# Optimization experiments

Measured on AMD Instinct MI355X. Metric: run time of the kernel, lower is better.

Reference implementation:

```python
import jax, jax.numpy as jnp
import numpy as np

BS, N, D, B, D_PM = 8, 4096, 1024, 8, 64
BUDGET = 16.0


def setup_inputs() -> dict:
    key = jax.random.key(0)
    ks = jax.random.split(key, 6)
    H = jax.random.normal(ks[0], (BS, N, D), jnp.float32)
    surprise = jax.random.normal(ks[1], (BS, N, D), jnp.float32)
    # W_pm initialized as (1/B)*I + small noise, as in initialize()
    eye = jnp.eye(D_PM, dtype=jnp.float32)
    W_pm = eye / B + 0.01 * jax.random.normal(ks[2], (BS, B, D_PM, D_PM), jnp.float32)
    proj_in_w = jax.random.normal(ks[3], (D_PM, D), jnp.float32) / np.float32(np.sqrt(D))
    proj_in_b = jnp.zeros((D_PM,), jnp.float32)
    # original zero-inits proj_out; use small values so output is non-trivial
    proj_out_w = 0.02 * jax.random.normal(ks[4], (D, D_PM), jnp.float32)
    proj_out_b = jnp.zeros((D,), jnp.float32)
    raw_beta = jnp.full((B,), -3.0, jnp.float32)
    raw_decay = jnp.full((B,), np.float32(np.log(0.999 / 0.001)), jnp.float32)  # logit(0.999)
    surp_scale = jnp.ones((1,), jnp.float32)
    surp_bias = jnp.zeros((1,), jnp.float32)
    return dict(H=H, surprise=surprise, W_pm=W_pm,
                proj_in_w=proj_in_w, proj_in_b=proj_in_b,
                proj_out_w=proj_out_w, proj_out_b=proj_out_b,
                raw_beta=raw_beta, raw_decay=raw_decay,
                surp_scale=surp_scale, surp_bias=surp_bias)


def reference(H, surprise, W_pm, proj_in_w, proj_in_b, proj_out_w, proj_out_b,
              raw_beta, raw_decay, surp_scale, surp_bias):
    # ---- read ----
    pre = jnp.einsum('bnd,pd->bnp', H, proj_in_w) + proj_in_b          # [BS,N,D_pm]
    W_sum = jnp.sum(W_pm, axis=1)                                      # [BS,D_pm,D_pm]
    post = jnp.einsum('bnp,bqp->bnq', pre, W_sum)                      # pre @ W_sum^T
    pm_read = jnp.einsum('bnq,dq->bnd', post, proj_out_w) + proj_out_b # [BS,N,D]
    # ---- commit (Hebbian, surprise-gated) ----
    surp_mag = jnp.linalg.norm(surprise, axis=-1)                      # [BS,N]
    s = jax.nn.sigmoid(surp_scale * surp_mag + surp_bias)              # [BS,N]
    weighted = jnp.sqrt(s)[..., None] * pre                            # [BS,N,D_pm]
    G = jnp.einsum('bnp,bnq->bpq', weighted, weighted) / N             # [BS,D_pm,D_pm]
    beta = jax.nn.softplus(raw_beta)                                   # [B]
    decay = jax.nn.sigmoid(raw_decay)                                  # [B]
    eye = jnp.eye(D_PM, dtype=pre.dtype)
    T = decay[None, :, None, None] * eye + beta[None, :, None, None] * G[:, None]  # [BS,B,D_pm,D_pm]
    W_new = jnp.einsum('bkij,bkjq->bkiq', W_pm, T)                     # [BS,B,D_pm,D_pm]
    frob = jnp.sqrt(jnp.sum(W_new * W_new, axis=(-2, -1), keepdims=True))
    scale = jnp.minimum(BUDGET / jnp.maximum(frob, 1e-8), 1.0)
    W_new = W_new * scale
    return pm_read, W_new
```

## Files before the change

### kernel.cpp

```cpp
#include <hip/hip_runtime.h>

typedef unsigned short u16;
typedef unsigned int u32;
typedef __attribute__((ext_vector_type(4))) float f32x4;
typedef __attribute__((ext_vector_type(8))) short s16x8;

static constexpr int N_ = 4096;
static constexpr int D_ = 1024;

#define WAITV(N) asm volatile("s_waitcnt vmcnt(" #N ")" ::: "memory")
#define MEMCLOB() asm volatile("" ::: "memory")

__device__ __forceinline__ u16 f2bf(float f) {
  unsigned u = __float_as_uint(f);
  u += 0x7FFFu + ((u >> 16) & 1u);
  return (u16)(u >> 16);
}

__device__ __forceinline__ f32x4 zero4() {
  f32x4 z; z[0] = 0.f; z[1] = 0.f; z[2] = 0.f; z[3] = 0.f; return z;
}

__device__ __forceinline__ void gload16(const void* g, void* lds) {
  __builtin_amdgcn_global_load_lds(
      (const __attribute__((address_space(1))) u32*)g,
      (__attribute__((address_space(3))) u32*)lds, 16, 0, 0);
}

__global__ __launch_bounds__(256) void k_aux(
    const float* __restrict__ Wpm, const float* __restrict__ piw,
    const float* __restrict__ pw, const float* __restrict__ Sur,
    const float* __restrict__ sscale_p, const float* __restrict__ sbias_p,
    u16* __restrict__ WpB, u16* __restrict__ MB, float* __restrict__ sqs_ws) {
  __shared__ float Ws[64][65];
  int bid = blockIdx.x, tid = threadIdx.x;
  if (bid < 16) {
    size_t i0 = (size_t)bid * 4096;
    for (int idx = tid; idx < 4096; idx += 256)
      WpB[i0 + idx] = f2bf(piw[i0 + idx]);
    return;
  }
  if (bid < 144) {
    int idx2 = bid - 16;
    int b = idx2 >> 4, t = idx2 & 15;
    for (int idx = tid; idx < 4096; idx += 256) {
      float s = 0.f;
#pragma unroll
      for (int k = 0; k < 8; ++k)
        s += Wpm[((size_t)(b * 8 + k)) * 4096 + idx];
      Ws[idx >> 6][idx & 63] = s;
    }
    __syncthreads();
    u16* mb = MB + ((size_t)b << 16);
    for (int oidx = tid; oidx < 4096; oidx += 256) {
      int r = oidx >> 6, c = oidx & 63;
      int drow = t * 64 + r;
      const float* prow = pw + (size_t)drow * 64;
      float acc = 0.f;
#pragma unroll 8
      for (int q = 0; q < 64; ++q) acc += prow[q] * Ws[q][c];
      mb[(size_t)drow * 64 + c] = f2bf(acc);
    }
    return;
  }
  int w = tid >> 6, lane = tid & 63;
  int fr = (bid - 144) * 16 + w * 4;
  const float4* r0 = (const float4*)(Sur + (size_t)fr * 1024) + lane;
  float s0 = 0.f, s1 = 0.f, s2 = 0.f, s3 = 0.f;
#pragma unroll
  for (int c = 0; c < 4; ++c) {
    float4 v0 = r0[c * 64];
    float4 v1 = r0[256 + c * 64];
    float4 v2 = r0[512 + c * 64];
    float4 v3 = r0[768 + c * 64];
    s0 += v0.x * v0.x + v0.y * v0.y + v0.z * v0.z + v0.w * v0.w;
    s1 += v1.x * v1.x + v1.y * v1.y + v1.z * v1.z + v1.w * v1.w;
    s2 += v2.x * v2.x + v2.y * v2.y + v2.z * v2.z + v2.w * v2.w;
    s3 += v3.x * v3.x + v3.y * v3.y + v3.z * v3.z + v3.w * v3.w;
  }
#pragma unroll
  for (int m = 1; m < 64; m <<= 1) {
    s0 += __shfl_xor(s0, m, 64);
    s1 += __shfl_xor(s1, m, 64);
    s2 += __shfl_xor(s2, m, 64);
    s3 += __shfl_xor(s3, m, 64);
  }
  float res = s0;
  if (lane == 1) res = s1;
  if (lane == 2) res = s2;
  if (lane == 3) res = s3;
  if (lane < 4) {
    float mag = sqrtf(res);
    float s = 1.f / (1.f + __expf(-(sscale_p[0] * mag + sbias_p[0])));
    sqs_ws[fr + lane] = sqrtf(s);
  }
}

__global__ __launch_bounds__(512, 4) void k_main(
    const float* __restrict__ H, const float* __restrict__ pib,
    const float* __restrict__ pob, const u16* __restrict__ WpB,
    const u16* __restrict__ MB, const float* __restrict__ sqs_ws,
    float* __restrict__ Gpart, float* __restrict__ out) {
  __shared__ __align__(16) char arena[32768];
  __shared__ __align__(16) u16 preRP[64][72];
  __shared__ __align__(16) u16 wRPT[64][72];
  __shared__ float pobL[1024];

  const int tid = threadIdx.x;
  const int lane = tid & 63;
  const int w = tid >> 6;
  const int wm = w & 3;
  const int wk = w >> 2;
  const int llo = lane & 15;
  const int lhi = lane >> 4;
  const int b = blockIdx.x >> 6;
  const int row0 = (blockIdx.x & 63) * 64;

  float bias_t[4];
#pragma unroll
  for (int t = 0; t < 4; ++t) bias_t[t] = pib[t * 16 + llo];
  float sqs_r[4];
#pragma unroll
  for (int r = 0; r < 4; ++r)
    sqs_r[r] = sqs_ws[b * 4096 + row0 + wm * 16 + lhi * 4 + r];

  const int srow = 8 * w + (lane >> 3);
  const int sc16 = (lane & 7) ^ (srow & 7);

  f32x4 accA[4];
#pragma unroll
  for (int t = 0; t < 4; ++t) accA[t] = zero4();

  const float* hsrc = H + ((size_t)b * N_ + row0 + srow) * D_ + sc16 * 4;
  const u16* wpb = WpB + (size_t)wk * 512 + lhi * 8;

  s16x8 B0[4], B1[4];
  auto LOADB = [&](int kc, s16x8* Bs) {
#pragma unroll
    for (int t = 0; t < 4; ++t)
      Bs[t] = *(const s16x8*)(wpb + (size_t)(t * 16 + llo) * 1024 + kc * 32);
  };
  auto STAGEH = [&](int kc, int buf) {
    gload16(hsrc + kc * 32, arena + buf * 16384 + w * 1024);
    gload16(hsrc + 512 + kc * 32, arena + buf * 16384 + 8192 + w * 1024);
  };
  const int arow = wm * 16 + llo;
  const int r7a = arow & 7;
  auto COMPA = [&](int buf, const s16x8* Bs) {
    const char* abase = arena + buf * 16384 + wk * 8192 + arow * 128;
    f32x4 alo = *(const f32x4*)(abase + (((lhi * 2) ^ r7a) * 16));
    f32x4 ahi = *(const f32x4*)(abase + (((lhi * 2 + 1) ^ r7a) * 16));
    s16x8 af;
    af[0] = (short)f2bf(alo[0]); af[1] = (short)f2bf(alo[1]);
    af[2] = (short)f2bf(alo[2]); af[3] = (short)f2bf(alo[3]);
    af[4] = (short)f2bf(ahi[0]); af[5] = (short)f2bf(ahi[1]);
    af[6] = (short)f2bf(ahi[2]); af[7] = (short)f2bf(ahi[3]);
#pragma unroll
    for (int t = 0; t < 4; ++t)
      accA[t] = __builtin_amdgcn_mfma_f32_16x16x32_bf16(af, Bs[t], accA[t], 0, 0, 0);
  };

  LOADB(0, B0); STAGEH(0, 0);
  MEMCLOB();
  LOADB(1, B1); STAGEH(1, 1);
  MEMCLOB();

  for (int kc = 0; kc < 16; kc += 2) {
    WAITV(6);
    __builtin_amdgcn_s_barrier();
    COMPA(0, B0);
    MEMCLOB();
    __builtin_amdgcn_s_barrier();
    if (kc + 2 < 16) { LOADB(kc + 2, B0); STAGEH(kc + 2, 0); }
    MEMCLOB();
    if (kc + 1 == 15) { WAITV(0); } else { WAITV(6); }
    __builtin_amdgcn_s_barrier();
    COMPA(1, B1);
    MEMCLOB();
    __builtin_amdgcn_s_barrier();
    if (kc + 3 < 16) { LOADB(kc + 3, B1); STAGEH(kc + 3, 1); }
    MEMCLOB();
  }

  __syncthreads();
  float (*preF)[65] = (float(*)[65])arena;
  if (wk == 1) {
#pragma unroll
    for (int t = 0; t < 4; ++t)
#pragma unroll
      for (int r = 0; r < 4; ++r)
        preF[wm * 16 + lhi * 4 + r][t * 16 + llo] = accA[t][r];
  }
  __syncthreads();
  if (wk == 0) {
#pragma unroll
    for (int t = 0; t < 4; ++t)
#pragma unroll
      for (int r = 0; r < 4; ++r) {
        int row = wm * 16 + lhi * 4 + r;
        float v = accA[t][r] + preF[row][t * 16 + llo] + bias_t[t];
        preRP[row][t * 16 + llo] = f2bf(v);
        wRPT[t * 16 + llo][row] = f2bf(v * sqs_r[r]);
      }
  }
  __syncthreads();

  {
    f32x4 accG[4];
#pragma unroll
    for (int t = 0; t < 4; ++t) accG[t] = zero4();
    s16x8 ag = *(const s16x8*)&wRPT[wm * 16 + llo][wk * 32 + lhi * 8];
#pragma unroll
    for (int t = 0; t < 4; ++t) {
      s16x8 bg = *(const s16x8*)&wRPT[t * 16 + llo][wk * 32 + lhi * 8];
      accG[t] = __builtin_amdgcn_mfma_f32_16x16x32_bf16(ag, bg, accG[t], 0, 0, 0);
    }
    float* gout = Gpart + ((size_t)blockIdx.x * 2 + wk) * 4096;
#pragma unroll
    for (int t = 0; t < 4; ++t)
#pragma unroll
      for (int r = 0; r < 4; ++r)
        gout[(wm * 16 + lhi * 4 + r) * 64 + t * 16 + llo] = accG[t][r];
  }

  pobL[tid] = pob[tid];
  pobL[tid + 512] = pob[tid + 512];
  __syncthreads();

  const u16* mbb = MB + ((size_t)b << 16);
  const u16* msrc0 = mbb + (size_t)srow * 64 + sc16 * 8;
  auto STAGED = [&](int c, int buf) {
    gload16(msrc0 + (size_t)c * 64 * 64, arena + buf * 16384 + w * 1024);
    gload16(msrc0 + (size_t)(512 + c * 64) * 64, arena + buf * 16384 + 8192 + w * 1024);
  };
  s16x8 ad0 = *(const s16x8*)&preRP[wm * 16 + llo][lhi * 8];
  s16x8 ad1 = *(const s16x8*)&preRP[wm * 16 + llo][32 + lhi * 8];
  float* orow = out + ((size_t)b * N_ + row0 + wm * 16) * D_;

  STAGED(0, 0);
  MEMCLOB();
  STAGED(1, 1);
  MEMCLOB();
  for (int c = 0; c < 8; ++c) {
    if (c == 0) { WAITV(2); }
    else if (c == 7) { WAITV(16); }
    else { WAITV(18); }
    __builtin_amdgcn_s_barrier();
    {
      const char* dbase = arena + (c & 1) * 16384 + wk * 8192;
#pragma unroll
      for (int i = 0; i < 4; ++i) {
        int row = i * 16 + llo;
        int r7 = row & 7;
        const char* base = dbase + row * 128;
        s16x8 b0 = *(const s16x8*)(base + ((lhi ^ r7) * 16));
        s16x8 b1 = *(const s16x8*)(base + (((4 + lhi) ^ r7) * 16));
        f32x4 acc = zero4();
        acc = __builtin_amdgcn_mfma_f32_16x16x32_bf16(ad0, b0, acc, 0, 0, 0);
        acc = __builtin_amdgcn_mfma_f32_16x16x32_bf16(ad1, b1, acc, 0, 0, 0);
        int n0 = wk * 512 + c * 64 + i * 16;
        float bias = pobL[n0 + llo];
#pragma unroll
        for (int r = 0; r < 4; ++r)
          orow[(size_t)(lhi * 4 + r) * D_ + n0 + llo] = acc[r] + bias;
      }
    }
    MEMCLOB();
    __builtin_amdgcn_s_barrier();
    if (c + 2 < 8) STAGED(c + 2, c & 1);
    MEMCLOB();
  }
}

__global__ __launch_bounds__(256) void k_wnew(
    const float* __restrict__ Wpm, const float* __restrict__ Gpart,
    const float* __restrict__ rbeta, const float* __restrict__ rdecay,
    float* __restrict__ outW) {
  __shared__ float Wk[64][68];
  __shared__ float Gl[64][68];
  __shared__ float red[4];
  int bk = blockIdx.x;
  int b = bk >> 3, k = bk & 7;
  int tid = threadIdx.x;
  f32x4 a0 = zero4(), a1 = zero4(), a2 = zero4(), a3 = zero4();
  const float* gp = Gpart + (size_t)b * 128 * 4096 + tid * 16;
#pragma unroll 2
  for (int sl = 0; sl < 128; ++sl) {
    const f32x4* p = (const f32x4*)(gp + (size_t)sl * 4096);
    a0 += p[0]; a1 += p[1]; a2 += p[2]; a3 += p[3];
  }
  {
    float* gl = &Gl[tid >> 2][(tid & 3) * 16];
#pragma unroll
    for (int j = 0; j < 4; ++j) {
      gl[j] = a0[j]; gl[4 + j] = a1[j]; gl[8 + j] = a2[j]; gl[12 + j] = a3[j];
    }
  }
  const float* wsrc = Wpm + (size_t)bk * 4096;
  for (int idx = tid; idx < 4096; idx += 256)
    Wk[idx >> 6][idx & 63] = wsrc[idx];
  __syncthreads();
  float beta = log1pf(__expf(rbeta[k]));
  float decay = 1.f / (1.f + __expf(-rdecay[k]));
  float bn = beta * (1.f / 4096.f);
  int q = tid & 63;
  int rbase = tid >> 6;
  float vals[16];
  float ss = 0.f;
#pragma unroll
  for (int i = 0; i < 16; ++i) {
    int row = i * 4 + rbase;
    float acc = 0.f;
#pragma unroll 8
    for (int j = 0; j < 64; ++j) acc += Wk[row][j] * Gl[j][q];
    float v = decay * Wk[row][q] + bn * acc;
    vals[i] = v;
    ss += v * v;
  }
#pragma unroll
  for (int m = 1; m < 64; m <<= 1) ss += __shfl_xor(ss, m, 64);
  if ((tid & 63) == 0) red[tid >> 6] = ss;
  __syncthreads();
  float frob = sqrtf(red[0] + red[1] + red[2] + red[3]);
  float scale = fminf(16.f / fmaxf(frob, 1e-8f), 1.f);
  float* dst = outW + (size_t)bk * 4096;
#pragma unroll
  for (int i = 0; i < 16; ++i) dst[i * 256 + tid] = vals[i] * scale;
}

extern "C" void kernel_launch(void* const* d_in, const int* in_sizes, int n_in,
                              void* d_out, int out_size, void* d_ws, size_t ws_size,
                              hipStream_t stream) {
  const float* H      = (const float*)d_in[0];
  const float* Sur    = (const float*)d_in[1];
  const float* Wpm    = (const float*)d_in[2];
  const float* piw    = (const float*)d_in[3];
  const float* pib    = (const float*)d_in[4];
  const float* pw     = (const float*)d_in[5];
  const float* pob    = (const float*)d_in[6];
  const float* rbeta  = (const float*)d_in[7];
  const float* rdecay = (const float*)d_in[8];
  const float* sscale = (const float*)d_in[9];
  const float* sbias  = (const float*)d_in[10];
  float* out = (float*)d_out;

  char* ws = (char*)d_ws;
  u16* WpB      = (u16*)(ws);
  u16* MB       = (u16*)(ws + 131072);
  float* sqs_ws = (float*)(ws + 1179648);
  float* Gpart  = (float*)(ws + 1310720);

  k_aux<<<2192, 256, 0, stream>>>(Wpm, piw, pw, Sur, sscale, sbias,
                                  WpB, MB, sqs_ws);
  k_main<<<512, 512, 0, stream>>>(H, pib, pob, WpB, MB, sqs_ws, Gpart, out);
  k_wnew<<<64, 256, 0, stream>>>(Wpm, Gpart, rbeta, rdecay,
                                 out + (size_t)8 * 4096 * 1024);
}
```

Measured before the change: 162.3 us.

## Fuse surprise norm into main kernel, deepen H pipeline, add parallel G reduction

```diff
diff --git a/kernel.cpp b/kernel.cpp
--- a/kernel.cpp
+++ b/kernel.cpp
@@ -29,9 +29,8 @@
 
 __global__ __launch_bounds__(256) void k_aux(
     const float* __restrict__ Wpm, const float* __restrict__ piw,
-    const float* __restrict__ pw, const float* __restrict__ Sur,
-    const float* __restrict__ sscale_p, const float* __restrict__ sbias_p,
-    u16* __restrict__ WpB, u16* __restrict__ MB, float* __restrict__ sqs_ws) {
+    const float* __restrict__ pw, u16* __restrict__ WpB,
+    u16* __restrict__ MB) {
   __shared__ float Ws[64][65];
   int bid = blockIdx.x, tid = threadIdx.x;
   if (bid < 16) {
@@ -40,71 +39,36 @@
       WpB[i0 + idx] = f2bf(piw[i0 + idx]);
     return;
   }
-  if (bid < 144) {
-    int idx2 = bid - 16;
-    int b = idx2 >> 4, t = idx2 & 15;
-    for (int idx = tid; idx < 4096; idx += 256) {
-      float s = 0.f;
-#pragma unroll
-      for (int k = 0; k < 8; ++k)
-        s += Wpm[((size_t)(b * 8 + k)) * 4096 + idx];
-      Ws[idx >> 6][idx & 63] = s;
-    }
-    __syncthreads();
-    u16* mb = MB + ((size_t)b << 16);
-    for (int oidx = tid; oidx < 4096; oidx += 256) {
-      int r = oidx >> 6, c = oidx & 63;
-      int drow = t * 64 + r;
-      const float* prow = pw + (size_t)drow * 64;
-      float acc = 0.f;
+  int idx2 = bid - 16;
+  int b = idx2 >> 4, t = idx2 & 15;
+  for (int idx = tid; idx < 4096; idx += 256) {
+    float s = 0.f;
+#pragma unroll
+    for (int k = 0; k < 8; ++k)
+      s += Wpm[((size_t)(b * 8 + k)) * 4096 + idx];
+    Ws[idx >> 6][idx & 63] = s;
+  }
+  __syncthreads();
+  u16* mb = MB + ((size_t)b << 16);
+  for (int oidx = tid; oidx < 4096; oidx += 256) {
+    int r = oidx >> 6, c = oidx & 63;
+    int drow = t * 64 + r;
+    const float* prow = pw + (size_t)drow * 64;
+    float acc = 0.f;
 #pragma unroll 8
-      for (int q = 0; q < 64; ++q) acc += prow[q] * Ws[q][c];
-      mb[(size_t)drow * 64 + c] = f2bf(acc);
-    }
-    return;
-  }
-  int w = tid >> 6, lane = tid & 63;
-  int fr = (bid - 144) * 16 + w * 4;
-  const float4* r0 = (const float4*)(Sur + (size_t)fr * 1024) + lane;
-  float s0 = 0.f, s1 = 0.f, s2 = 0.f, s3 = 0.f;
-#pragma unroll
-  for (int c = 0; c < 4; ++c) {
-    float4 v0 = r0[c * 64];
-    float4 v1 = r0[256 + c * 64];
-    float4 v2 = r0[512 + c * 64];
-    float4 v3 = r0[768 + c * 64];
-    s0 += v0.x * v0.x + v0.y * v0.y + v0.z * v0.z + v0.w * v0.w;
-    s1 += v1.x * v1.x + v1.y * v1.y + v1.z * v1.z + v1.w * v1.w;
-    s2 += v2.x * v2.x + v2.y * v2.y + v2.z * v2.z + v2.w * v2.w;
-    s3 += v3.x * v3.x + v3.y * v3.y + v3.z * v3.z + v3.w * v3.w;
-  }
-#pragma unroll
-  for (int m = 1; m < 64; m <<= 1) {
-    s0 += __shfl_xor(s0, m, 64);
-    s1 += __shfl_xor(s1, m, 64);
-    s2 += __shfl_xor(s2, m, 64);
-    s3 += __shfl_xor(s3, m, 64);
-  }
-  float res = s0;
-  if (lane == 1) res = s1;
-  if (lane == 2) res = s2;
-  if (lane == 3) res = s3;
-  if (lane < 4) {
-    float mag = sqrtf(res);
-    float s = 1.f / (1.f + __expf(-(sscale_p[0] * mag + sbias_p[0])));
-    sqs_ws[fr + lane] = sqrtf(s);
+    for (int q = 0; q < 64; ++q) acc += prow[q] * Ws[q][c];
+    mb[(size_t)drow * 64 + c] = f2bf(acc);
   }
 }
 
 __global__ __launch_bounds__(512, 4) void k_main(
-    const float* __restrict__ H, const float* __restrict__ pib,
-    const float* __restrict__ pob, const u16* __restrict__ WpB,
-    const u16* __restrict__ MB, const float* __restrict__ sqs_ws,
+    const float* __restrict__ H, const float* __restrict__ Sur,
+    const float* __restrict__ pib, const float* __restrict__ pob,
+    const float* __restrict__ sscale_p, const float* __restrict__ sbias_p,
+    const u16* __restrict__ WpB, const u16* __restrict__ MB,
     float* __restrict__ Gpart, float* __restrict__ out) {
-  __shared__ __align__(16) char arena[32768];
-  __shared__ __align__(16) u16 preRP[64][72];
-  __shared__ __align__(16) u16 wRPT[64][72];
-  __shared__ float pobL[1024];
+  __shared__ __align__(16) char arena[65536];
+  __shared__ float sqsL[64];
 
   const int tid = threadIdx.x;
   const int lane = tid & 63;
@@ -116,74 +80,107 @@
   const int b = blockIdx.x >> 6;
   const int row0 = (blockIdx.x & 63) * 64;
 
-  float bias_t[4];
-#pragma unroll
-  for (int t = 0; t < 4; ++t) bias_t[t] = pib[t * 16 + llo];
-  float sqs_r[4];
-#pragma unroll
-  for (int r = 0; r < 4; ++r)
-    sqs_r[r] = sqs_ws[b * 4096 + row0 + wm * 16 + lhi * 4 + r];
+  {
+    const float* sb = Sur + ((size_t)b * N_ + row0) * D_;
+    const float sscale = sscale_p[0], sbias = sbias_p[0];
+#pragma unroll
+    for (int g = 0; g < 2; ++g) {
+      const float4* r0 = (const float4*)(sb + (size_t)(w * 8 + g * 4) * D_) + lane;
+      float s0 = 0.f, s1 = 0.f, s2 = 0.f, s3 = 0.f;
+#pragma unroll
+      for (int c = 0; c < 4; ++c) {
+        float4 v0 = r0[c * 64];
+        float4 v1 = r0[256 + c * 64];
+        float4 v2 = r0[512 + c * 64];
+        float4 v3 = r0[768 + c * 64];
+        s0 += v0.x * v0.x + v0.y * v0.y + v0.z * v0.z + v0.w * v0.w;
+        s1 += v1.x * v1.x + v1.y * v1.y + v1.z * v1.z + v1.w * v1.w;
+        s2 += v2.x * v2.x + v2.y * v2.y + v2.z * v2.z + v2.w * v2.w;
+        s3 += v3.x * v3.x + v3.y * v3.y + v3.z * v3.z + v3.w * v3.w;
+      }
+#pragma unroll
+      for (int m = 1; m < 64; m <<= 1) {
+        s0 += __shfl_xor(s0, m, 64);
+        s1 += __shfl_xor(s1, m, 64);
+        s2 += __shfl_xor(s2, m, 64);
+        s3 += __shfl_xor(s3, m, 64);
+      }
+      float res = s0;
+      if (lane == 1) res = s1;
+      if (lane == 2) res = s2;
+      if (lane == 3) res = s3;
+      if (lane < 4) {
+        float mag = sqrtf(res);
+        float s = 1.f / (1.f + __expf(-(sscale * mag + sbias)));
+        sqsL[w * 8 + g * 4 + lane] = sqrtf(s);
+      }
+    }
+  }
+  __syncthreads();
 
   const int srow = 8 * w + (lane >> 3);
   const int sc16 = (lane & 7) ^ (srow & 7);
-
-  f32x4 accA[4];
-#pragma unroll
-  for (int t = 0; t < 4; ++t) accA[t] = zero4();
-
   const float* hsrc = H + ((size_t)b * N_ + row0 + srow) * D_ + sc16 * 4;
   const u16* wpb = WpB + (size_t)wk * 512 + lhi * 8;
 
-  s16x8 B0[4], B1[4];
-  auto LOADB = [&](int kc, s16x8* Bs) {
-#pragma unroll
-    for (int t = 0; t < 4; ++t)
-      Bs[t] = *(const s16x8*)(wpb + (size_t)(t * 16 + llo) * 1024 + kc * 32);
-  };
-  auto STAGEH = [&](int kc, int buf) {
-    gload16(hsrc + kc * 32, arena + buf * 16384 + w * 1024);
-    gload16(hsrc + 512 + kc * 32, arena + buf * 16384 + 8192 + w * 1024);
-  };
+  f32x4 accA[4];
+#pragma unroll
+  for (int t = 0; t < 4; ++t) accA[t] = zero4();
+  s16x8 Bf[2][4];
+
   const int arow = wm * 16 + llo;
   const int r7a = arow & 7;
-  auto COMPA = [&](int buf, const s16x8* Bs) {
-    const char* abase = arena + buf * 16384 + wk * 8192 + arow * 128;
-    f32x4 alo = *(const f32x4*)(abase + (((lhi * 2) ^ r7a) * 16));
-    f32x4 ahi = *(const f32x4*)(abase + (((lhi * 2 + 1) ^ r7a) * 16));
-    s16x8 af;
-    af[0] = (short)f2bf(alo[0]); af[1] = (short)f2bf(alo[1]);
-    af[2] = (short)f2bf(alo[2]); af[3] = (short)f2bf(alo[3]);
-    af[4] = (short)f2bf(ahi[0]); af[5] = (short)f2bf(ahi[1]);
-    af[6] = (short)f2bf(ahi[2]); af[7] = (short)f2bf(ahi[3]);
-#pragma unroll
-    for (int t = 0; t < 4; ++t)
-      accA[t] = __builtin_amdgcn_mfma_f32_16x16x32_bf16(af, Bs[t], accA[t], 0, 0, 0);
-  };
-
-  LOADB(0, B0); STAGEH(0, 0);
+
+#define STAGEH(kc)                                                          \
+  gload16(hsrc + (kc) * 32, arena + ((kc) & 3) * 16384 + w * 1024);         \
+  gload16(hsrc + 512 + (kc) * 32, arena + ((kc) & 3) * 16384 + 8192 + w * 1024)
+
+#define LOADB(kc)                                                           \
+  _Pragma("unroll") for (int t = 0; t < 4; ++t) Bf[(kc) & 1][t] =           \
+      *(const s16x8*)(wpb + (size_t)(t * 16 + llo) * 1024 + (kc) * 32)
+
+  STAGEH(0); STAGEH(1); STAGEH(2);
+  LOADB(0); LOADB(1);
   MEMCLOB();
-  LOADB(1, B1); STAGEH(1, 1);
-  MEMCLOB();
-
-  for (int kc = 0; kc < 16; kc += 2) {
-    WAITV(6);
+
+#pragma unroll
+  for (int kc = 0; kc < 16; ++kc) {
+    if (kc <= 13) { WAITV(12); }
+    else if (kc == 14) { WAITV(8); }
+    else { WAITV(0); }
     __builtin_amdgcn_s_barrier();
-    COMPA(0, B0);
     MEMCLOB();
-    __builtin_amdgcn_s_barrier();
-    if (kc + 2 < 16) { LOADB(kc + 2, B0); STAGEH(kc + 2, 0); }
+    {
+      const char* abase = arena + (kc & 3) * 16384 + wk * 8192 + arow * 128;
+      f32x4 alo = *(const f32x4*)(abase + (((lhi * 2) ^ r7a) * 16));
+      f32x4 ahi = *(const f32x4*)(abase + (((lhi * 2 + 1) ^ r7a) * 16));
+      s16x8 af;
+      af[0] = (short)f2bf(alo[0]); af[1] = (short)f2bf(alo[1]);
+      af[2] = (short)f2bf(alo[2]); af[3] = (short)f2bf(alo[3]);
+      af[4] = (short)f2bf(ahi[0]); af[5] = (short)f2bf(ahi[1]);
+      af[6] = (short)f2bf(ahi[2]); af[7] = (short)f2bf(ahi[3]);
+#pragma unroll
+      for (int t = 0; t < 4; ++t)
+        accA[t] = __builtin_amdgcn_mfma_f32_16x16x32_bf16(af, Bf[kc & 1][t],
+                                                          accA[t], 0, 0, 0);
+    }
+    if (kc + 2 < 16) { LOADB(kc + 2); }
+    if (kc + 3 < 16) { STAGEH(kc + 3); }
     MEMCLOB();
-    if (kc + 1 == 15) { WAITV(0); } else { WAITV(6); }
-    __builtin_amdgcn_s_barrier();
-    COMPA(1, B1);
-    MEMCLOB();
-    __builtin_amdgcn_s_barrier();
-    if (kc + 3 < 16) { LOADB(kc + 3, B1); STAGEH(kc + 3, 1); }
-    MEMCLOB();
-  }
+  }
+#undef STAGEH
+#undef LOADB
+
+  float bias_t[4];
+#pragma unroll
+  for (int t = 0; t < 4; ++t) bias_t[t] = pib[t * 16 + llo];
 
   __syncthreads();
   float (*preF)[65] = (float(*)[65])arena;
+  u16 (*preRP)[72] = (u16(*)[72])(arena + 18432);
+  u16 (*wRPT)[72] = (u16(*)[72])(arena + 28672);
+  float* pobL = (float*)(arena + 38912);
+
   if (wk == 1) {
 #pragma unroll
     for (int t = 0; t < 4; ++t)
@@ -200,7 +197,7 @@
         int row = wm * 16 + lhi * 4 + r;
         float v = accA[t][r] + preF[row][t * 16 + llo] + bias_t[t];
         preRP[row][t * 16 + llo] = f2bf(v);
-        wRPT[t * 16 + llo][row] = f2bf(v * sqs_r[r]);
+        wRPT[t * 16 + llo][row] = f2bf(v * sqsL[row]);
       }
   }
   __syncthreads();
@@ -222,42 +219,29 @@
       for (int r = 0; r < 4; ++r)
         gout[(wm * 16 + lhi * 4 + r) * 64 + t * 16 + llo] = accG[t][r];
   }
-
   pobL[tid] = pob[tid];
   pobL[tid + 512] = pob[tid + 512];
   __syncthreads();
 
-  const u16* mbb = MB + ((size_t)b << 16);
-  const u16* msrc0 = mbb + (size_t)srow * 64 + sc16 * 8;
-  auto STAGED = [&](int c, int buf) {
-    gload16(msrc0 + (size_t)c * 64 * 64, arena + buf * 16384 + w * 1024);
-    gload16(msrc0 + (size_t)(512 + c * 64) * 64, arena + buf * 16384 + 8192 + w * 1024);
-  };
-  s16x8 ad0 = *(const s16x8*)&preRP[wm * 16 + llo][lhi * 8];
-  s16x8 ad1 = *(const s16x8*)&preRP[wm * 16 + llo][32 + lhi * 8];
-  float* orow = out + ((size_t)b * N_ + row0 + wm * 16) * D_;
-
-  STAGED(0, 0);
-  MEMCLOB();
-  STAGED(1, 1);
-  MEMCLOB();
-  for (int c = 0; c < 8; ++c) {
-    if (c == 0) { WAITV(2); }
-    else if (c == 7) { WAITV(16); }
-    else { WAITV(18); }
-    __builtin_amdgcn_s_barrier();
-    {
-      const char* dbase = arena + (c & 1) * 16384 + wk * 8192;
+  {
+    s16x8 ad0 = *(const s16x8*)&preRP[wm * 16 + llo][lhi * 8];
+    s16x8 ad1 = *(const s16x8*)&preRP[wm * 16 + llo][32 + lhi * 8];
+    const u16* mcol = MB + ((size_t)b << 16) + (size_t)(wk * 512) * 64 + lhi * 8;
+    float* orow = out + ((size_t)b * N_ + row0 + wm * 16) * D_;
+#pragma unroll
+    for (int c = 0; c < 8; ++c) {
+      s16x8 f0[4], f1[4];
 #pragma unroll
       for (int i = 0; i < 4; ++i) {
-        int row = i * 16 + llo;
-        int r7 = row & 7;
-        const char* base = dbase + row * 128;
-        s16x8 b0 = *(const s16x8*)(base + ((lhi ^ r7) * 16));
-        s16x8 b1 = *(const s16x8*)(base + (((4 + lhi) ^ r7) * 16));
+        const u16* p = mcol + (size_t)(c * 64 + i * 16 + llo) * 64;
+        f0[i] = *(const s16x8*)p;
+        f1[i] = *(const s16x8*)(p + 32);
+      }
+#pragma unroll
+      for (int i = 0; i < 4; ++i) {
         f32x4 acc = zero4();
-        acc = __builtin_amdgcn_mfma_f32_16x16x32_bf16(ad0, b0, acc, 0, 0, 0);
-        acc = __builtin_amdgcn_mfma_f32_16x16x32_bf16(ad1, b1, acc, 0, 0, 0);
+        acc = __builtin_amdgcn_mfma_f32_16x16x32_bf16(ad0, f0[i], acc, 0, 0, 0);
+        acc = __builtin_amdgcn_mfma_f32_16x16x32_bf16(ad1, f1[i], acc, 0, 0, 0);
         int n0 = wk * 512 + c * 64 + i * 16;
         float bias = pobL[n0 + llo];
 #pragma unroll
@@ -265,40 +249,41 @@
           orow[(size_t)(lhi * 4 + r) * D_ + n0 + llo] = acc[r] + bias;
       }
     }
-    MEMCLOB();
-    __builtin_amdgcn_s_barrier();
-    if (c + 2 < 8) STAGED(c + 2, c & 1);
-    MEMCLOB();
-  }
+  }
+}
+
+__global__ __launch_bounds__(256) void k_gred(
+    const float* __restrict__ Gpart, float* __restrict__ Gsum) {
+  __shared__ float red[4][64];
+  int b = blockIdx.x >> 6, g = blockIdx.x & 63;
+  int lane = threadIdx.x & 63, q = threadIdx.x >> 6;
+  const float* src = Gpart + ((size_t)b * 128 + q * 32) * 4096 + g * 64 + lane;
+  float s = 0.f;
+#pragma unroll 8
+  for (int i = 0; i < 32; ++i) s += src[(size_t)i * 4096];
+  red[q][lane] = s;
+  __syncthreads();
+  if (q == 0)
+    Gsum[(size_t)b * 4096 + g * 64 + lane] =
+        red[0][lane] + red[1][lane] + red[2][lane] + red[3][lane];
 }
 
 __global__ __launch_bounds__(256) void k_wnew(
-    const float* __restrict__ Wpm, const float* __restrict__ Gpart,
+    const float* __restrict__ Wpm, const float* __restrict__ Gsum,
     const float* __restrict__ rbeta, const float* __restrict__ rdecay,
     float* __restrict__ outW) {
-  __shared__ float Wk[64][68];
-  __shared__ float Gl[64][68];
+  __shared__ float Wk[64][66];
+  __shared__ float Gl[64][66];
   __shared__ float red[4];
   int bk = blockIdx.x;
   int b = bk >> 3, k = bk & 7;
   int tid = threadIdx.x;
-  f32x4 a0 = zero4(), a1 = zero4(), a2 = zero4(), a3 = zero4();
-  const float* gp = Gpart + (size_t)b * 128 * 4096 + tid * 16;
-#pragma unroll 2
-  for (int sl = 0; sl < 128; ++sl) {
-    const f32x4* p = (const f32x4*)(gp + (size_t)sl * 4096);
-    a0 += p[0]; a1 += p[1]; a2 += p[2]; a3 += p[3];
-  }
-  {
-    float* gl = &Gl[tid >> 2][(tid & 3) * 16];
-#pragma unroll
-    for (int j = 0; j < 4; ++j) {
-      gl[j] = a0[j]; gl[4 + j] = a1[j]; gl[8 + j] = a2[j]; gl[12 + j] = a3[j];
-    }
-  }
   const float* wsrc = Wpm + (size_t)bk * 4096;
-  for (int idx = tid; idx < 4096; idx += 256)
+  const float* gsrc = Gsum + (size_t)b * 4096;
+  for (int idx = tid; idx < 4096; idx += 256) {
     Wk[idx >> 6][idx & 63] = wsrc[idx];
+    Gl[idx >> 6][idx & 63] = gsrc[idx];
+  }
   __syncthreads();
   float beta = log1pf(__expf(rbeta[k]));
   float decay = 1.f / (1.f + __expf(-rdecay[k]));
@@ -345,14 +330,15 @@
   float* out = (float*)d_out;
 
   char* ws = (char*)d_ws;
-  u16* WpB      = (u16*)(ws);
-  u16* MB       = (u16*)(ws + 131072);
-  float* sqs_ws = (float*)(ws + 1179648);
-  float* Gpart  = (float*)(ws + 1310720);
-
-  k_aux<<<2192, 256, 0, stream>>>(Wpm, piw, pw, Sur, sscale, sbias,
-                                  WpB, MB, sqs_ws);
-  k_main<<<512, 512, 0, stream>>>(H, pib, pob, WpB, MB, sqs_ws, Gpart, out);
-  k_wnew<<<64, 256, 0, stream>>>(Wpm, Gpart, rbeta, rdecay,
+  u16* WpB     = (u16*)(ws);
+  u16* MB      = (u16*)(ws + 131072);
+  float* Gsum  = (float*)(ws + 1179648);
+  float* Gpart = (float*)(ws + 1310720);
+
+  k_aux<<<144, 256, 0, stream>>>(Wpm, piw, pw, WpB, MB);
+  k_main<<<512, 512, 0, stream>>>(H, Sur, pib, pob, sscale, sbias,
+                                  WpB, MB, Gpart, out);
+  k_gred<<<512, 256, 0, stream>>>(Gpart, Gsum);
+  k_wnew<<<64, 256, 0, stream>>>(Wpm, Gsum, rbeta, rdecay,
                                  out + (size_t)8 * 4096 * 1024);
 }
```

Measured after the change: 164.6 us. About the same (+1.4%).
